# Kernel tuning notes

Measured on AMD Instinct MI355X. Metric: run time of the kernel, lower is better.

The kernel has to match this reference:

```python
import jax, jax.numpy as jnp
import numpy as np
from jax import lax

BITWIDTH = 7
EPS = 1e-5


def ti_quant(x):
    """TiFloatToInt8: per-tensor int8 quantization with power-of-2 scale."""
    rng = jnp.max(jnp.abs(x))
    bw = jnp.ceil(jnp.log2(rng))
    exp = bw - BITWIDTH
    q = jnp.clip(jnp.round(x * 2.0 ** (BITWIDTH - bw)), -128.0, 127.0)
    return q, exp


def ti_conv(xv, xe, wv, we, pad):
    """TiConv2d: integer conv (simulated in f32, all values int-valued),
    int32 accumulate, then shift back to 8 bits; exponents add."""
    acc = lax.conv_general_dilated(
        xv, wv, window_strides=(1, 1), padding=[(pad, pad), (pad, pad)],
        dimension_numbers=("NCHW", "OIHW", "NCHW"))
    rng = jnp.max(jnp.abs(acc))
    bw = jnp.ceil(jnp.log2(rng))
    shift = jnp.maximum(bw - BITWIDTH, 0.0)
    q = jnp.clip(jnp.round(acc * 2.0 ** (-shift)), -128.0, 127.0)
    return q, xe + we + shift


def batchnorm(x, gamma, beta):
    # training-mode BN: batch statistics over (N, H, W)
    mean = jnp.mean(x, axis=(0, 2, 3), keepdims=True)
    var = jnp.var(x, axis=(0, 2, 3), keepdims=True)
    g = gamma[None, :, None, None]
    b = beta[None, :, None, None]
    return g * (x - mean) * lax.rsqrt(var + EPS) + b


def setup_inputs() -> dict:
    key = jax.random.key(0)
    k0, k1, k2, k3, k4 = jax.random.split(key, 5)
    B, Cin, Cout, H, W = 32, 128, 256, 56, 56
    x_val = jax.random.randint(k0, (B, Cin, H, W), -128, 128, dtype=jnp.int32)
    x_exp = jnp.zeros((), jnp.float32) - 7.0
    wDW = jnp.round(jnp.clip(jax.random.normal(k1, (Cin, Cin, 3, 3), jnp.float32) * 32.0, -128.0, 127.0))
    wDW_exp = jnp.zeros((), jnp.float32) - 9.0
    wPW = jnp.round(jnp.clip(jax.random.normal(k2, (Cout, Cin, 1, 1), jnp.float32) * 32.0, -128.0, 127.0))
    wPW_exp = jnp.zeros((), jnp.float32) - 9.0
    gamma1 = jnp.ones((Cin,), jnp.float32) + 0.1 * jax.random.normal(k3, (Cin,), jnp.float32)
    beta1 = jnp.zeros((Cin,), jnp.float32)
    gamma2 = jnp.ones((Cout,), jnp.float32) + 0.1 * jax.random.normal(k4, (Cout,), jnp.float32)
    beta2 = jnp.zeros((Cout,), jnp.float32)
    return {"x_val": x_val, "x_exp": x_exp, "wDW": wDW, "wDW_exp": wDW_exp,
            "wPW": wPW, "wPW_exp": wPW_exp, "gamma1": gamma1, "beta1": beta1,
            "gamma2": gamma2, "beta2": beta2}


def reference(x_val, x_exp, wDW, wDW_exp, wPW, wPW_exp, gamma1, beta1, gamma2, beta2):
    xv = x_val.astype(jnp.float32)
    # convDW (3x3, in->in, pad=1)
    q, e = ti_conv(xv, x_exp, wDW, wDW_exp, 1)
    # dequant -> bn1 -> quant
    f = batchnorm(q * 2.0 ** e, gamma1, beta1)
    q, e = ti_quant(f)
    # TiReLU on int values
    q = jnp.maximum(q, 0.0)
    # convPW (1x1, in->out)
    q, e = ti_conv(q, e, wPW, wPW_exp, 0)
    # dequant -> bn2 -> quant -> relu
    f = batchnorm(q * 2.0 ** e, gamma2, beta2)
    q, e = ti_quant(f)
    q = jnp.maximum(q, 0.0)
    return q.astype(jnp.int8), e
```

## Files before the change

kernel.cpp:

```cpp
#include <hip/hip_runtime.h>
#include <cstdint>
#include <cstddef>

#define C1 128
#define C2 256
#define Hh 56
#define Wd 56
#define HW 3136
#define NHW 100352
#define N1 ((size_t)12845056)
#define N2 ((size_t)25690112)
#define XPSZ ((size_t)13778944)

typedef int v4i __attribute__((ext_vector_type(4)));
typedef int v16i __attribute__((ext_vector_type(16)));

static constexpr size_t OFF_XP = 0;
static constexpr size_t OFF_Q1 = XPSZ;
static constexpr size_t OFF_Q3 = OFF_Q1 + N1;
static constexpr size_t OFF_WQ1 = OFF_Q3 + N2;
static constexpr size_t OFF_WQ2 = OFF_WQ1 + 147456;
static constexpr size_t OFF_STATS = OFF_WQ2 + 32768;

struct Stats {
  int absmax1, absmax2, pad0, pad1;
  float scale1, e1, s2, e2;
  float scaleq2, e3, sf, ef;
  int sum1[C1]; unsigned sumsq1[C1];
  int min1[C1], max1[C1];
  float A1[C1], B1c[C1];
  int sum2[C2]; unsigned sumsq2[C2];
  int min2[C2], max2[C2];
  float A2[C2], B2c[C2];
};

__global__ void k_init(Stats* st) {
  int t = threadIdx.x;
  if (t == 0) { st->absmax1 = 0; st->absmax2 = 0; }
  for (int c = t; c < C1; c += 256) {
    st->sum1[c] = 0; st->sumsq1[c] = 0; st->min1[c] = 127; st->max1[c] = -128;
  }
  for (int c = t; c < C2; c += 256) {
    st->sum2[c] = 0; st->sumsq2[c] = 0; st->min2[c] = 127; st->max2[c] = -128;
  }
}

__global__ __launch_bounds__(256) void k_prep_x2(
    const int* __restrict__ x, signed char* __restrict__ xp) {
  __shared__ signed char lds[56 * 132];
  int t = threadIdx.x;
  int hh = blockIdx.x;
  int n = blockIdx.y;
  int* xpw = (int*)(xp + ((size_t)n * 58 + hh) * 7424);
  if (hh == 0 || hh == 57) {
    for (int o = t; o < 1856; o += 256) xpw[o] = 0;
    return;
  }
  int h = hh - 1;
  const int* xb = x + (size_t)n * C1 * HW + h * 56;
  for (int idx = t; idx < 7168; idx += 256) {
    int c = idx / 56, w = idx - c * 56;
    lds[w * 132 + c] = (signed char)xb[(size_t)c * HW + w];
  }
  __syncthreads();
  for (int o = t; o < 1856; o += 256) {
    int kb = o / 232, r = o - kb * 232, ww = r >> 2, cw = r & 3;
    int val = (ww == 0 || ww == 57) ? 0
              : *(const int*)&lds[(ww - 1) * 132 + kb * 16 + cw * 4];
    xpw[o] = val;
  }
}

__global__ void k_prep_w1(const float* __restrict__ wDW, signed char* __restrict__ wq1t) {
  int idx = blockIdx.x * 256 + threadIdx.x;
  if (idx >= 128 * 1152) return;
  int co = idx / 1152, r = idx - co * 1152;
  int ci = r / 9, pos = r - ci * 9;
  int k = pos * 128 + ci;
  wq1t[(size_t)(k >> 4) * 2048 + co * 16 + (k & 15)] = (signed char)(int)wDW[idx];
}

__global__ void k_prep_w2(const float* __restrict__ wPW, signed char* __restrict__ wq2t) {
  int i = blockIdx.x * 256 + threadIdx.x;
  int co = i >> 7, ci = i & 127;
  wq2t[(size_t)(ci >> 4) * 4096 + co * 16 + (ci & 15)] = (signed char)(int)wPW[i];
}

__global__ void k_scale(const int* __restrict__ absmax_p,
                        const float* __restrict__ ea, const float* __restrict__ eb,
                        float* scale_out, float* e_out) {
  int v = *absmax_p;
  int p = 31 - __clz(v | 1);
  int bw = ((v & (v - 1)) == 0) ? p : p + 1;
  int shift = bw - 7; if (shift < 0) shift = 0;
  *scale_out = exp2f((float)(-shift));
  *e_out = *ea + *eb + (float)shift;
}

__device__ inline v4i ld16_lds(const signed char* p) {
  const int2* q = (const int2*)p;
  int2 lo = q[0], hi = q[1];
  v4i r; r[0] = lo.x; r[1] = lo.y; r[2] = hi.x; r[3] = hi.y;
  return r;
}

template <int STORE>
__global__ __launch_bounds__(256, 2) void k_conv1t(
    const signed char* __restrict__ xp, const signed char* __restrict__ wq1t,
    signed char* __restrict__ q1, Stats* st) {
  __shared__ int qti[256 * 34];
  __shared__ int psum[C1], psq[C1], pmn[C1], pmx[C1];
  __shared__ int reda[4];
  signed char* qt = (signed char*)qti;

  int t = threadIdx.x, lane = t & 63, wave = t >> 6;
  int half = lane >> 5, l31 = lane & 31;
  size_t g0 = (size_t)blockIdx.x * 256;

  const signed char* ab[2];
#pragma unroll
  for (int i = 0; i < 2; ++i) {
    size_t gm = g0 + wave * 64 + i * 32 + l31;
    int n = (int)(gm / HW);
    int p = (int)(gm - (size_t)n * HW);
    int h = p / 56, w = p - h * 56;
    ab[i] = xp + ((size_t)n * 58 + h) * 7424 + w * 16 + half * 928;
  }
  const signed char* bb[4];
#pragma unroll
  for (int j = 0; j < 4; ++j)
    bb[j] = wq1t + (size_t)(j * 32 + l31) * 16 + half * 2048;

  v16i a1[2][4];
#pragma unroll
  for (int i = 0; i < 2; ++i)
#pragma unroll
    for (int j = 0; j < 4; ++j)
#pragma unroll
      for (int r = 0; r < 16; ++r) a1[i][j][r] = 0;

#pragma unroll
  for (int pos = 0; pos < 9; ++pos) {
    int kh = pos / 3, kw = pos - kh * 3;
    const signed char* a0p = ab[0] + kh * 7424 + kw * 16;
    const signed char* a1p = ab[1] + kh * 7424 + kw * 16;
#pragma unroll
    for (int kb = 0; kb < 8; kb += 2) {
      v4i af0 = *(const v4i*)(a0p + kb * 928);
      v4i af1 = *(const v4i*)(a1p + kb * 928);
      v4i bf[4];
#pragma unroll
      for (int j = 0; j < 4; ++j)
        bf[j] = *(const v4i*)(bb[j] + pos * 16384 + kb * 2048);
#pragma unroll
      for (int j = 0; j < 4; ++j) {
        a1[0][j] = __builtin_amdgcn_mfma_i32_32x32x32_i8(af0, bf[j], a1[0][j], 0, 0, 0);
        a1[1][j] = __builtin_amdgcn_mfma_i32_32x32x32_i8(af1, bf[j], a1[1][j], 0, 0, 0);
      }
    }
  }

  if (STORE == 0) {
    int am = 0;
#pragma unroll
    for (int i = 0; i < 2; ++i)
#pragma unroll
      for (int j = 0; j < 4; ++j)
#pragma unroll
        for (int r = 0; r < 16; ++r) am = max(am, abs(a1[i][j][r]));
    for (int off = 32; off; off >>= 1) am = max(am, __shfl_down(am, off, 64));
    if (lane == 0) reda[wave] = am;
    __syncthreads();
    if (t == 0)
      atomicMax(&st->absmax1, max(max(reda[0], reda[1]), max(reda[2], reda[3])));
  } else {
    if (t < C1) { psum[t] = 0; psq[t] = 0; pmn[t] = 127; pmx[t] = -128; }
    __syncthreads();
    float scale1 = st->scale1;
#pragma unroll
    for (int j = 0; j < 4; ++j) {
      int sj = 0, sqj = 0, mnj = 127, mxj = -128;
      int c = j * 32 + l31;
#pragma unroll
      for (int i = 0; i < 2; ++i)
#pragma unroll
        for (int reg = 0; reg < 16; ++reg) {
          int row = (reg & 3) + 8 * (reg >> 2) + 4 * half;
          int pix = wave * 64 + i * 32 + row;
          float r = rintf((float)a1[i][j][reg] * scale1);
          r = fminf(fmaxf(r, -128.f), 127.f);
          int qi = (int)r;
          qt[pix * 136 + c] = (signed char)qi;
          sj += qi; sqj += qi * qi; mnj = min(mnj, qi); mxj = max(mxj, qi);
        }
      sj += __shfl_down(sj, 32, 64);
      sqj += __shfl_down(sqj, 32, 64);
      mnj = min(mnj, __shfl_down(mnj, 32, 64));
      mxj = max(mxj, __shfl_down(mxj, 32, 64));
      if (half == 0) {
        atomicAdd(&psum[c], sj); atomicAdd(&psq[c], sqj);
        atomicMin(&pmn[c], mnj); atomicMax(&pmx[c], mxj);
      }
    }
    __syncthreads();
    if (t < C1) {
      atomicAdd(&st->sum1[t], psum[t]);
      atomicAdd(&st->sumsq1[t], (unsigned)psq[t]);
      atomicMin(&st->min1[t], pmn[t]);
      atomicMax(&st->max1[t], pmx[t]);
    }
    int* q1w = (int*)(q1 + g0 * 128);
    for (int idx = t; idx < 8192; idx += 256) {
      int pix = idx >> 5, c4 = idx & 31;
      q1w[idx] = qti[pix * 34 + c4];
    }
  }
}

template <int STORE>
__global__ __launch_bounds__(256, 2) void k_conv2t(
    const signed char* __restrict__ q1, const signed char* __restrict__ wq2t,
    signed char* __restrict__ q3, Stats* st) {
  __shared__ int qti[128 * 34];
  __shared__ signed char stg[128 * 264];
  __shared__ int psum[C2], psq[C2], pmn[C2], pmx[C2];
  __shared__ int reda[4];
  signed char* qt = (signed char*)qti;

  int t = threadIdx.x, lane = t & 63, wave = t >> 6;
  int half = lane >> 5, l31 = lane & 31;
  size_t g0 = (size_t)blockIdx.x * 128;

  if (STORE) { psum[t] = 0; psq[t] = 0; pmn[t] = 127; pmx[t] = -128; }

  int c4 = t & 31;
  float Av[4], Bv[4];
#pragma unroll
  for (int jj = 0; jj < 4; ++jj) {
    Av[jj] = st->A1[c4 * 4 + jj];
    Bv[jj] = st->B1c[c4 * 4 + jj];
  }
  float s2 = st->s2;
  const int* q1w = (const int*)(q1 + g0 * 128);
#pragma unroll
  for (int k = 0; k < 16; ++k) {
    int idx = k * 256 + t;
    int v = q1w[idx];
    int pix = idx >> 5;
    int outv = 0;
#pragma unroll
    for (int jj = 0; jj < 4; ++jj) {
      int b = (signed char)(v >> (8 * jj));
      float y = Av[jj] * (float)b + Bv[jj];
      float r = rintf(y * s2);
      r = fminf(fmaxf(r, -128.f), 127.f);
      r = fmaxf(r, 0.f);
      outv |= ((int)r & 0xff) << (8 * jj);
    }
    qti[pix * 34 + c4] = outv;
  }
  __syncthreads();

  v16i acc[8];
#pragma unroll
  for (int j = 0; j < 8; ++j)
#pragma unroll
    for (int r = 0; r < 16; ++r) acc[j][r] = 0;

#pragma unroll
  for (int ks = 0; ks < 4; ++ks) {
    v4i af = ld16_lds(&qt[(wave * 32 + l31) * 136 + half * 16 + ks * 32]);
#pragma unroll
    for (int j = 0; j < 8; ++j) {
      v4i bf = *(const v4i*)(wq2t + (size_t)(ks * 2 + half) * 4096 + (j * 32 + l31) * 16);
      acc[j] = __builtin_amdgcn_mfma_i32_32x32x32_i8(af, bf, acc[j], 0, 0, 0);
    }
  }

  if (STORE == 0) {
    int am2 = 0;
#pragma unroll
    for (int j = 0; j < 8; ++j)
#pragma unroll
      for (int r = 0; r < 16; ++r) am2 = max(am2, abs(acc[j][r]));
    for (int off = 32; off; off >>= 1) am2 = max(am2, __shfl_down(am2, off, 64));
    if (lane == 0) reda[wave] = am2;
    __syncthreads();
    if (t == 0)
      atomicMax(&st->absmax2, max(max(reda[0], reda[1]), max(reda[2], reda[3])));
  } else {
    float scale2 = st->scaleq2;
#pragma unroll
    for (int j = 0; j < 8; ++j) {
      int c = j * 32 + l31;
      int sj = 0, sqj = 0, mnj = 127, mxj = -128;
#pragma unroll
      for (int reg = 0; reg < 16; ++reg) {
        int row = (reg & 3) + 8 * (reg >> 2) + 4 * half;
        float r = rintf((float)acc[j][reg] * scale2);
        r = fminf(fmaxf(r, -128.f), 127.f);
        int qi = (int)r;
        stg[(wave * 32 + row) * 264 + c] = (signed char)qi;
        sj += qi; sqj += qi * qi; mnj = min(mnj, qi); mxj = max(mxj, qi);
      }
      sj += __shfl_down(sj, 32, 64);
      sqj += __shfl_down(sqj, 32, 64);
      mnj = min(mnj, __shfl_down(mnj, 32, 64));
      mxj = max(mxj, __shfl_down(mxj, 32, 64));
      if (half == 0) {
        atomicAdd(&psum[c], sj); atomicAdd(&psq[c], sqj);
        atomicMin(&pmn[c], mnj); atomicMax(&pmx[c], mxj);
      }
    }
    __syncthreads();
    atomicAdd(&st->sum2[t], psum[t]);
    atomicAdd(&st->sumsq2[t], (unsigned)psq[t]);
    atomicMin(&st->min2[t], pmn[t]);
    atomicMax(&st->max2[t], pmx[t]);
    int* q3w = (int*)(q3 + g0 * 256);
#pragma unroll
    for (int k = 0; k < 32; ++k) {
      int idx = k * 256 + t;
      int pix = idx >> 6, cw = idx & 63;
      q3w[idx] = *(const int*)&stg[pix * 264 + cw * 4];
    }
  }
}

__global__ void k_bn(const int* __restrict__ sums,
                     const unsigned* __restrict__ sumsqs,
                     const int* __restrict__ mins, const int* __restrict__ maxs,
                     const float* __restrict__ gamma, const float* __restrict__ beta,
                     const float* __restrict__ e_in,
                     float* A, float* Bc, float* s_out, float* e_out,
                     float* e_extra, int C) {
  __shared__ float red[4];
  int t = threadIdx.x;
  float e1 = *e_in;
  double meanq = (double)sums[t] / (double)NHW;
  double varq = (double)sumsqs[t] / (double)NHW - meanq * meanq;
  float se = exp2f(e1);
  float mean = (float)meanq * se;
  float var = (float)varq * se * se;
  float rsq = 1.0f / sqrtf(var + 1e-5f);
  float g = gamma[t], b = beta[t];
  float Avv = g * se * rsq;
  float Bvv = b - g * mean * rsq;
  A[t] = Avv; Bc[t] = Bvv;
  float cand = fmaxf(fabsf(Avv * (float)mins[t] + Bvv), fabsf(Avv * (float)maxs[t] + Bvv));
  for (int off = 32; off; off >>= 1) cand = fmaxf(cand, __shfl_down(cand, off, 64));
  int wave = t >> 6, lane = t & 63;
  if (lane == 0) red[wave] = cand;
  __syncthreads();
  if (t == 0) {
    float rng = red[0];
    for (int i = 1; i < C / 64; i++) rng = fmaxf(rng, red[i]);
    float bwv = ceilf(log2f(rng));
    *s_out = exp2f(7.0f - bwv);
    *e_out = bwv - 7.0f;
    if (e_extra) *e_extra = bwv - 7.0f;
  }
}

__global__ __launch_bounds__(256) void k_out(
    const signed char* __restrict__ q3, const Stats* __restrict__ st,
    float* __restrict__ out) {
  int t = threadIdx.x, lane = t & 63, wave = t >> 6;
  int nb = blockIdx.x;
  int n = nb / 49, p0 = (nb - n * 49) * 64;
  const int* q3w = (const int*)(q3 + ((size_t)n * HW + p0) * 256);
  float sf = st->sf;
  float* ob = out + (size_t)n * C2 * HW + p0 + lane;
#pragma unroll
  for (int i = 0; i < 16; ++i) {
    int cg2 = wave * 16 + i;
    int v = q3w[(size_t)lane * 64 + cg2];
#pragma unroll
    for (int j = 0; j < 4; ++j) {
      int c = cg2 * 4 + j;
      float y = st->A2[c] * (float)((signed char)(v >> (8 * j))) + st->B2c[c];
      float r = rintf(y * sf);
      r = fminf(fmaxf(r, -128.f), 127.f);
      ob[(size_t)c * HW] = fmaxf(r, 0.f);
    }
  }
}

extern "C" void kernel_launch(void* const* d_in, const int* in_sizes, int n_in,
                              void* d_out, int out_size, void* d_ws, size_t ws_size,
                              hipStream_t stream) {
  const int* x = (const int*)d_in[0];
  const float* x_exp = (const float*)d_in[1];
  const float* wDW = (const float*)d_in[2];
  const float* wDW_exp = (const float*)d_in[3];
  const float* wPW = (const float*)d_in[4];
  const float* wPW_exp = (const float*)d_in[5];
  const float* gamma1 = (const float*)d_in[6];
  const float* beta1 = (const float*)d_in[7];
  const float* gamma2 = (const float*)d_in[8];
  const float* beta2 = (const float*)d_in[9];
  float* out = (float*)d_out;

  char* ws = (char*)d_ws;
  signed char* xp2 = (signed char*)(ws + OFF_XP);
  signed char* q1 = (signed char*)(ws + OFF_Q1);
  signed char* q3 = (signed char*)(ws + OFF_Q3);
  signed char* wq1t = (signed char*)(ws + OFF_WQ1);
  signed char* wq2t = (signed char*)(ws + OFF_WQ2);
  Stats* st = (Stats*)(ws + OFF_STATS);

  hipLaunchKernelGGL(k_init, dim3(1), dim3(256), 0, stream, st);
  hipLaunchKernelGGL(k_prep_x2, dim3(58, 32), dim3(256), 0, stream, x, xp2);
  hipLaunchKernelGGL(k_prep_w1, dim3(576), dim3(256), 0, stream, wDW, wq1t);
  hipLaunchKernelGGL(k_prep_w2, dim3(128), dim3(256), 0, stream, wPW, wq2t);

  hipLaunchKernelGGL(k_conv1t<0>, dim3(392), dim3(256), 0, stream,
                     xp2, wq1t, q1, st);
  hipLaunchKernelGGL(k_scale, dim3(1), dim3(1), 0, stream,
                     &st->absmax1, x_exp, wDW_exp, &st->scale1, &st->e1);
  hipLaunchKernelGGL(k_conv1t<1>, dim3(392), dim3(256), 0, stream,
                     xp2, wq1t, q1, st);
  hipLaunchKernelGGL(k_bn, dim3(1), dim3(C1), 0, stream,
                     st->sum1, st->sumsq1, st->min1, st->max1, gamma1, beta1,
                     &st->e1, st->A1, st->B1c, &st->s2, &st->e2, (float*)nullptr, C1);

  hipLaunchKernelGGL(k_conv2t<0>, dim3(784), dim3(256), 0, stream,
                     q1, wq2t, q3, st);
  hipLaunchKernelGGL(k_scale, dim3(1), dim3(1), 0, stream,
                     &st->absmax2, &st->e2, wPW_exp, &st->scaleq2, &st->e3);
  hipLaunchKernelGGL(k_conv2t<1>, dim3(784), dim3(256), 0, stream,
                     q1, wq2t, q3, st);
  hipLaunchKernelGGL(k_bn, dim3(1), dim3(C2), 0, stream,
                     st->sum2, st->sumsq2, st->min2, st->max2, gamma2, beta2,
                     &st->e3, st->A2, st->B2c, &st->sf, &st->ef, out + N2, C2);
  hipLaunchKernelGGL(k_out, dim3(1568), dim3(256), 0, stream, q3, st, out);
}
```

Before: 315.7 us.

## Spill conv1 int32 accumulators instead of recomputing conv1, fold scale kernels

The 3x3 conv used to run twice, once for the absmax and once for quantization. It now runs once and writes its int32 accumulators to a new workspace buffer in fragment order, and a separate kernel reads them back to quantize and gather BN statistics. The tiny k_scale kernels are removed and the shift/scale computation is inlined into the consumer kernels. k_out now stages q3 through LDS so that global reads are coalesced. This trades a second pass of MFMA compute for about 51MB of extra int32 write and read traffic.

```diff
diff --git a/kernel.cpp b/kernel.cpp
--- a/kernel.cpp
+++ b/kernel.cpp
@@ -16,7 +16,8 @@
 typedef int v16i __attribute__((ext_vector_type(16)));
 
 static constexpr size_t OFF_XP = 0;
-static constexpr size_t OFF_Q1 = XPSZ;
+static constexpr size_t OFF_ACC1 = XPSZ;
+static constexpr size_t OFF_Q1 = OFF_ACC1 + 4 * N1;
 static constexpr size_t OFF_Q3 = OFF_Q1 + N1;
 static constexpr size_t OFF_WQ1 = OFF_Q3 + N2;
 static constexpr size_t OFF_WQ2 = OFF_WQ1 + 147456;
@@ -86,17 +87,6 @@
   wq2t[(size_t)(ci >> 4) * 4096 + co * 16 + (ci & 15)] = (signed char)(int)wPW[i];
 }
 
-__global__ void k_scale(const int* __restrict__ absmax_p,
-                        const float* __restrict__ ea, const float* __restrict__ eb,
-                        float* scale_out, float* e_out) {
-  int v = *absmax_p;
-  int p = 31 - __clz(v | 1);
-  int bw = ((v & (v - 1)) == 0) ? p : p + 1;
-  int shift = bw - 7; if (shift < 0) shift = 0;
-  *scale_out = exp2f((float)(-shift));
-  *e_out = *ea + *eb + (float)shift;
-}
-
 __device__ inline v4i ld16_lds(const signed char* p) {
   const int2* q = (const int2*)p;
   int2 lo = q[0], hi = q[1];
@@ -104,15 +94,10 @@
   return r;
 }
 
-template <int STORE>
-__global__ __launch_bounds__(256, 2) void k_conv1t(
+__global__ __launch_bounds__(256, 2) void k_conv1s(
     const signed char* __restrict__ xp, const signed char* __restrict__ wq1t,
-    signed char* __restrict__ q1, Stats* st) {
-  __shared__ int qti[256 * 34];
-  __shared__ int psum[C1], psq[C1], pmn[C1], pmx[C1];
+    int* __restrict__ acc1, Stats* st) {
   __shared__ int reda[4];
-  signed char* qt = (signed char*)qti;
-
   int t = threadIdx.x, lane = t & 63, wave = t >> 6;
   int half = lane >> 5, l31 = lane & 31;
   size_t g0 = (size_t)blockIdx.x * 256;
@@ -160,67 +145,94 @@
     }
   }
 
-  if (STORE == 0) {
-    int am = 0;
+  int am = 0;
+#pragma unroll
+  for (int i = 0; i < 2; ++i)
+#pragma unroll
+    for (int j = 0; j < 4; ++j)
+#pragma unroll
+      for (int r = 0; r < 16; ++r) am = max(am, abs(a1[i][j][r]));
+  for (int off = 32; off; off >>= 1) am = max(am, __shfl_down(am, off, 64));
+  if (lane == 0) reda[wave] = am;
+  __syncthreads();
+  if (t == 0)
+    atomicMax(&st->absmax1, max(max(reda[0], reda[1]), max(reda[2], reda[3])));
+
+  int* ob = acc1 + (size_t)blockIdx.x * 32768;
+#pragma unroll
+  for (int i = 0; i < 2; ++i)
+#pragma unroll
+    for (int j = 0; j < 4; ++j)
+#pragma unroll
+      for (int reg = 0; reg < 16; ++reg)
+        ob[(((wave * 2 + i) * 4 + j) * 16 + reg) * 64 + lane] = a1[i][j][reg];
+}
+
+__global__ __launch_bounds__(256, 2) void k_qstats1(
+    const int* __restrict__ acc1, signed char* __restrict__ q1, Stats* st,
+    const float* __restrict__ x_exp, const float* __restrict__ wDW_exp) {
+  __shared__ int qti[256 * 34];
+  __shared__ int psum[C1], psq[C1], pmn[C1], pmx[C1];
+  signed char* qt = (signed char*)qti;
+  int t = threadIdx.x, lane = t & 63, wave = t >> 6;
+  int half = lane >> 5, l31 = lane & 31;
+
+  if (t < C1) { psum[t] = 0; psq[t] = 0; pmn[t] = 127; pmx[t] = -128; }
+  __syncthreads();
+
+  int v1 = st->absmax1;
+  int pw = 31 - __clz(v1 | 1);
+  int bw = ((v1 & (v1 - 1)) == 0) ? pw : pw + 1;
+  int sh = max(bw - 7, 0);
+  float scale1 = exp2f((float)(-sh));
+  if (blockIdx.x == 0 && t == 0)
+    st->e1 = x_exp[0] + wDW_exp[0] + (float)sh;
+
+  const int* ib = acc1 + (size_t)blockIdx.x * 32768;
+#pragma unroll
+  for (int j = 0; j < 4; ++j) {
+    int sj = 0, sqj = 0, mnj = 127, mxj = -128;
+    int c = j * 32 + l31;
 #pragma unroll
     for (int i = 0; i < 2; ++i)
 #pragma unroll
-      for (int j = 0; j < 4; ++j)
-#pragma unroll
-        for (int r = 0; r < 16; ++r) am = max(am, abs(a1[i][j][r]));
-    for (int off = 32; off; off >>= 1) am = max(am, __shfl_down(am, off, 64));
-    if (lane == 0) reda[wave] = am;
-    __syncthreads();
-    if (t == 0)
-      atomicMax(&st->absmax1, max(max(reda[0], reda[1]), max(reda[2], reda[3])));
-  } else {
-    if (t < C1) { psum[t] = 0; psq[t] = 0; pmn[t] = 127; pmx[t] = -128; }
-    __syncthreads();
-    float scale1 = st->scale1;
-#pragma unroll
-    for (int j = 0; j < 4; ++j) {
-      int sj = 0, sqj = 0, mnj = 127, mxj = -128;
-      int c = j * 32 + l31;
-#pragma unroll
-      for (int i = 0; i < 2; ++i)
-#pragma unroll
-        for (int reg = 0; reg < 16; ++reg) {
-          int row = (reg & 3) + 8 * (reg >> 2) + 4 * half;
-          int pix = wave * 64 + i * 32 + row;
-          float r = rintf((float)a1[i][j][reg] * scale1);
-          r = fminf(fmaxf(r, -128.f), 127.f);
-          int qi = (int)r;
-          qt[pix * 136 + c] = (signed char)qi;
-          sj += qi; sqj += qi * qi; mnj = min(mnj, qi); mxj = max(mxj, qi);
-        }
-      sj += __shfl_down(sj, 32, 64);
-      sqj += __shfl_down(sqj, 32, 64);
-      mnj = min(mnj, __shfl_down(mnj, 32, 64));
-      mxj = max(mxj, __shfl_down(mxj, 32, 64));
-      if (half == 0) {
-        atomicAdd(&psum[c], sj); atomicAdd(&psq[c], sqj);
-        atomicMin(&pmn[c], mnj); atomicMax(&pmx[c], mxj);
+      for (int reg = 0; reg < 16; ++reg) {
+        int av = ib[(((wave * 2 + i) * 4 + j) * 16 + reg) * 64 + lane];
+        int row = (reg & 3) + 8 * (reg >> 2) + 4 * half;
+        int pix = wave * 64 + i * 32 + row;
+        float r = rintf((float)av * scale1);
+        r = fminf(fmaxf(r, -128.f), 127.f);
+        int qi = (int)r;
+        qt[pix * 136 + c] = (signed char)qi;
+        sj += qi; sqj += qi * qi; mnj = min(mnj, qi); mxj = max(mxj, qi);
       }
-    }
-    __syncthreads();
-    if (t < C1) {
-      atomicAdd(&st->sum1[t], psum[t]);
-      atomicAdd(&st->sumsq1[t], (unsigned)psq[t]);
-      atomicMin(&st->min1[t], pmn[t]);
-      atomicMax(&st->max1[t], pmx[t]);
-    }
-    int* q1w = (int*)(q1 + g0 * 128);
-    for (int idx = t; idx < 8192; idx += 256) {
-      int pix = idx >> 5, c4 = idx & 31;
-      q1w[idx] = qti[pix * 34 + c4];
-    }
+    sj += __shfl_down(sj, 32, 64);
+    sqj += __shfl_down(sqj, 32, 64);
+    mnj = min(mnj, __shfl_down(mnj, 32, 64));
+    mxj = max(mxj, __shfl_down(mxj, 32, 64));
+    if (half == 0) {
+      atomicAdd(&psum[c], sj); atomicAdd(&psq[c], sqj);
+      atomicMin(&pmn[c], mnj); atomicMax(&pmx[c], mxj);
+    }
+  }
+  __syncthreads();
+  if (t < C1) {
+    atomicAdd(&st->sum1[t], psum[t]);
+    atomicAdd(&st->sumsq1[t], (unsigned)psq[t]);
+    atomicMin(&st->min1[t], pmn[t]);
+    atomicMax(&st->max1[t], pmx[t]);
+  }
+  int* q1w = (int*)(q1 + (size_t)blockIdx.x * 256 * 128);
+  for (int idx = t; idx < 8192; idx += 256) {
+    int pix = idx >> 5, c4 = idx & 31;
+    q1w[idx] = qti[pix * 34 + c4];
   }
 }
 
 template <int STORE>
 __global__ __launch_bounds__(256, 2) void k_conv2t(
     const signed char* __restrict__ q1, const signed char* __restrict__ wq2t,
-    signed char* __restrict__ q3, Stats* st) {
+    signed char* __restrict__ q3, Stats* st, const float* __restrict__ wPW_exp) {
   __shared__ int qti[128 * 34];
   __shared__ signed char stg[128 * 264];
   __shared__ int psum[C2], psq[C2], pmn[C2], pmx[C2];
@@ -289,7 +301,13 @@
     if (t == 0)
       atomicMax(&st->absmax2, max(max(reda[0], reda[1]), max(reda[2], reda[3])));
   } else {
-    float scale2 = st->scaleq2;
+    int v2 = st->absmax2;
+    int pw = 31 - __clz(v2 | 1);
+    int bw = ((v2 & (v2 - 1)) == 0) ? pw : pw + 1;
+    int sh2 = max(bw - 7, 0);
+    float scale2 = exp2f((float)(-sh2));
+    if (blockIdx.x == 0 && t == 0)
+      st->e3 = st->e2 + wPW_exp[0] + (float)sh2;
 #pragma unroll
     for (int j = 0; j < 8; ++j) {
       int c = j * 32 + l31;
@@ -365,20 +383,27 @@
 __global__ __launch_bounds__(256) void k_out(
     const signed char* __restrict__ q3, const Stats* __restrict__ st,
     float* __restrict__ out) {
+  __shared__ signed char lds[64 * 260];
   int t = threadIdx.x, lane = t & 63, wave = t >> 6;
-  int nb = blockIdx.x;
-  int n = nb / 49, p0 = (nb - n * 49) * 64;
-  const int* q3w = (const int*)(q3 + ((size_t)n * HW + p0) * 256);
+  size_t g0 = (size_t)blockIdx.x * 64;
+  int n = (int)(g0 / HW), p0 = (int)(g0 - (size_t)n * HW);
+  const int* q3w = (const int*)(q3 + g0 * 256);
+#pragma unroll
+  for (int k = 0; k < 16; ++k) {
+    int idx = k * 256 + t;
+    int pix = idx >> 6, cw = idx & 63;
+    *(int*)&lds[pix * 260 + cw * 4] = q3w[idx];
+  }
+  __syncthreads();
   float sf = st->sf;
   float* ob = out + (size_t)n * C2 * HW + p0 + lane;
 #pragma unroll
-  for (int i = 0; i < 16; ++i) {
-    int cg2 = wave * 16 + i;
-    int v = q3w[(size_t)lane * 64 + cg2];
-#pragma unroll
-    for (int j = 0; j < 4; ++j) {
-      int c = cg2 * 4 + j;
-      float y = st->A2[c] * (float)((signed char)(v >> (8 * j))) + st->B2c[c];
+  for (int cg = 0; cg < 16; ++cg) {
+    int v = *(const int*)&lds[lane * 260 + wave * 64 + cg * 4];
+#pragma unroll
+    for (int jj = 0; jj < 4; ++jj) {
+      int c = wave * 64 + cg * 4 + jj;
+      float y = st->A2[c] * (float)((signed char)(v >> (8 * jj))) + st->B2c[c];
       float r = rintf(y * sf);
       r = fminf(fmaxf(r, -128.f), 127.f);
       ob[(size_t)c * HW] = fmaxf(r, 0.f);
@@ -403,6 +428,7 @@
 
   char* ws = (char*)d_ws;
   signed char* xp2 = (signed char*)(ws + OFF_XP);
+  int* acc1 = (int*)(ws + OFF_ACC1);
   signed char* q1 = (signed char*)(ws + OFF_Q1);
   signed char* q3 = (signed char*)(ws + OFF_Q3);
   signed char* wq1t = (signed char*)(ws + OFF_WQ1);
@@ -414,22 +440,18 @@
   hipLaunchKernelGGL(k_prep_w1, dim3(576), dim3(256), 0, stream, wDW, wq1t);
   hipLaunchKernelGGL(k_prep_w2, dim3(128), dim3(256), 0, stream, wPW, wq2t);
 
-  hipLaunchKernelGGL(k_conv1t<0>, dim3(392), dim3(256), 0, stream,
-                     xp2, wq1t, q1, st);
-  hipLaunchKernelGGL(k_scale, dim3(1), dim3(1), 0, stream,
-                     &st->absmax1, x_exp, wDW_exp, &st->scale1, &st->e1);
-  hipLaunchKernelGGL(k_conv1t<1>, dim3(392), dim3(256), 0, stream,
-                     xp2, wq1t, q1, st);
+  hipLaunchKernelGGL(k_conv1s, dim3(392), dim3(256), 0, stream,
+                     xp2, wq1t, acc1, st);
+  hipLaunchKernelGGL(k_qstats1, dim3(392), dim3(256), 0, stream,
+                     acc1, q1, st, x_exp, wDW_exp);
   hipLaunchKernelGGL(k_bn, dim3(1), dim3(C1), 0, stream,
                      st->sum1, st->sumsq1, st->min1, st->max1, gamma1, beta1,
                      &st->e1, st->A1, st->B1c, &st->s2, &st->e2, (float*)nullptr, C1);
 
   hipLaunchKernelGGL(k_conv2t<0>, dim3(784), dim3(256), 0, stream,
-                     q1, wq2t, q3, st);
-  hipLaunchKernelGGL(k_scale, dim3(1), dim3(1), 0, stream,
-                     &st->absmax2, &st->e2, wPW_exp, &st->scaleq2, &st->e3);
+                     q1, wq2t, q3, st, wPW_exp);
   hipLaunchKernelGGL(k_conv2t<1>, dim3(784), dim3(256), 0, stream,
-                     q1, wq2t, q3, st);
+                     q1, wq2t, q3, st, wPW_exp);
   hipLaunchKernelGGL(k_bn, dim3(1), dim3(C2), 0, stream,
                      st->sum2, st->sumsq2, st->min2, st->max2, gamma2, beta2,
                      &st->e3, st->A2, st->B2c, &st->sf, &st->ef, out + N2, C2);
```

Result: faster. 297.7 us (-5.7%).
